# Performance work log

Hardware: AMD Instinct MI355X
Metric: run time of the kernel (lower is better)

Reference implementation:

```python
import jax, jax.numpy as jnp
import numpy as np

N_HIDDEN = 128
N_HEAD = 8
DIM_HEAD = N_HIDDEN // N_HEAD


def setup_inputs() -> dict:
    key = jax.random.key(0)
    ks = jax.random.split(key, 16)
    B, N, H = 2, 512, N_HIDDEN
    x = jax.random.normal(ks[0], (B, N, H), dtype=jnp.float32)
    e = jax.random.normal(ks[1], (B, N, N, H), dtype=jnp.float32)
    attention_mask = jnp.zeros((B, 1, N, N), dtype=jnp.float32)
    s = 1.0 / np.sqrt(H)
    def lin(kw, kb):
        W = jax.random.normal(kw, (H, H), dtype=jnp.float32) * s
        b = jax.random.normal(kb, (H,), dtype=jnp.float32) * s
        return W, b
    Wq, bq = lin(ks[2], ks[3])
    Wk, bk = lin(ks[4], ks[5])
    We, be = lin(ks[6], ks[7])
    Woh, boh = lin(ks[8], ks[9])
    Woe, boe = lin(ks[10], ks[11])
    return {"x": x, "e": e, "attention_mask": attention_mask,
            "Wq": Wq, "bq": bq, "Wk": Wk, "bk": bk,
            "We": We, "be": be, "Woh": Woh, "boh": boh,
            "Woe": Woe, "boe": boe}


def reference(x, e, attention_mask, Wq, bq, Wk, bk, We, be, Woh, boh, Woe, boe):
    B, N, H = x.shape
    h, dh = N_HEAD, DIM_HEAD
    # Projections -> [B, h, N, dh]
    Qx = (x @ Wq + bq).reshape(B, N, h, dh).transpose(0, 2, 1, 3)
    Kx = (x @ Wk + bk).reshape(B, N, h, dh).transpose(0, 2, 1, 3)
    Vx = Kx  # faithful to original: V_x = self.K(x)
    # Edge projection -> [B, h, N, N, dh]
    Ee = (e @ We + be).reshape(B, N, N, h, dh).transpose(0, 3, 1, 2, 4)
    # Elementwise Q*K*E biased scores: [B, h, N, N, dh]
    inter = Qx[:, :, :, None, :] * Kx[:, :, None, :, :] * Ee / np.sqrt(dh).astype(np.float32)
    scores = jax.nn.softmax(attention_mask + inter.sum(-1), axis=-1)  # [B, h, N, N]
    # Edge output: [B, N, N, H] -> Oe (dropout is identity at eval)
    e_out = inter.transpose(0, 2, 3, 1, 4).reshape(B, N, N, H) @ Woe + boe
    # Node output
    att = jnp.einsum('bhij,bhjd->bhid', scores, Vx)  # [B, h, N, dh]
    x_out = att.transpose(0, 2, 1, 3).reshape(B, N, H) @ Woh + boh
    return (x_out, e_out, scores)
```

## Files before the change

### kernel.cpp

```cpp
#include <hip/hip_runtime.h>
#include <hip/hip_bf16.h>


#define NB 2
#define NN 512
#define NHID 128
#define BQ 32

typedef __bf16 bf16x8 __attribute__((ext_vector_type(8)));
typedef __bf16 bf16x4 __attribute__((ext_vector_type(4)));
typedef float  f32x4  __attribute__((ext_vector_type(4)));
typedef float  vf4    __attribute__((ext_vector_type(4)));

union U16 { uint4 u; bf16x8 v; };

#define BAR_LGKM() do {                                          \
    asm volatile("s_waitcnt lgkmcnt(0)" ::: "memory");           \
    __builtin_amdgcn_sched_barrier(0);                           \
    __builtin_amdgcn_s_barrier();                                \
    __builtin_amdgcn_sched_barrier(0);                           \
} while (0)

__device__ __forceinline__ void swizzle_ib(int L, int& i, int& b) {
    const int Lp = (L & 7) * 128 + (L >> 3);
    b = Lp >> 9;
    i = Lp & 511;
}

__global__ __launch_bounds__(128)
void proj_kernel(const float* __restrict__ x,
                 const float* __restrict__ Wq, const float* __restrict__ bq,
                 const float* __restrict__ Wk, const float* __restrict__ bk,
                 float* __restrict__ Qhat, float* __restrict__ Khat)
{
    const int row = blockIdx.x;
    const int c   = threadIdx.x;
    __shared__ float xs[NHID];
    xs[c] = x[(long)row*NHID + c];
    __syncthreads();
    float q = bq[c], k = bk[c];
    #pragma unroll 8
    for (int kk = 0; kk < NHID; ++kk) {
        const float xv = xs[kk];
        q += xv * Wq[kk*NHID + c];
        k += xv * Wk[kk*NHID + c];
    }
    Qhat[(long)row*NHID + c] = q;
    Khat[(long)row*NHID + c] = k;
}

__global__ __launch_bounds__(128)
void wcvt_kernel(const float* __restrict__ We, const float* __restrict__ Woe,
                 __bf16* __restrict__ WeT, __bf16* __restrict__ WoeT)
{
    const int cb = blockIdx.x;
    const int k  = threadIdx.x;
    if (cb < NHID) {
        WeT[cb*NHID + k] = (__bf16)We[k*NHID + cb];
    } else {
        const int c = cb - NHID;
        WoeT[c*NHID + k] = (__bf16)Woe[k*NHID + c];
    }
}

__global__ __launch_bounds__(256, 4)
void mha_main(const float* __restrict__ e,
              const float* __restrict__ be,
              const float* __restrict__ boe,
              const float* __restrict__ Qhat,
              const float* __restrict__ Khat,
              const __bf16* __restrict__ WeT,
              const __bf16* __restrict__ WoeT,
              float* __restrict__ eout,
              float* __restrict__ sout)
{
    int i, b;
    swizzle_ib(blockIdx.y*NN + blockIdx.x, i, b);
    const int tid = threadIdx.x;
    const int w   = tid >> 6;
    const int l   = tid & 63;
    const int l15 = l & 15;
    const int lg  = l >> 4;
    const int wcol = w * 32;

    __shared__ __align__(16) __bf16 Elds[2][BQ*NHID];
    __shared__ __align__(16) __bf16 Mlds[BQ*NHID];

    const long rowbi = (long)b*NN + i;
    const float* Esrc = e    + rowbi*(long)(NN*NHID);
    float*       Edst = eout + rowbi*(long)(NN*NHID);
    const float* Kb   = Khat + (long)b*NN*NHID;

    float qv[2], bev[2], boev[2];
    bf16x8 fWe[2][4], fWoe[2][4];
    #pragma unroll
    for (int ct = 0; ct < 2; ++ct) {
        const int c = wcol + ct*16 + l15;
        qv[ct]   = Qhat[rowbi*NHID + c] * 0.25f;
        bev[ct]  = be[c];
        boev[ct] = boe[c];
        #pragma unroll
        for (int ks = 0; ks < 4; ++ks) {
            const int kb = ks*32 + lg*8;
            U16 ua, ub;
            ua.u = *(const uint4*)(WeT  + c*NHID + kb);
            ub.u = *(const uint4*)(WoeT + c*NHID + kb);
            fWe[ct][ks]  = ua.v;
            fWoe[ct][ks] = ub.v;
        }
    }
    const bool selp[4] = { (0*2 + (lg>>1)) == l15, (1*2 + (lg>>1)) == l15,
                           (2*2 + (lg>>1)) == l15, (3*2 + (lg>>1)) == l15 };

    vf4 rf[4];
    {
        const vf4* src = (const vf4*)Esrc;
        #pragma unroll
        for (int it = 0; it < 4; ++it)
            rf[it] = __builtin_nontemporal_load(&src[it*256 + tid]);
        #pragma unroll
        for (int it = 0; it < 4; ++it) {
            const int L = (it*256 + tid)*4;
            const int row = L >> 7, k = L & 127;
            bf16x4 v;
            v[0]=(__bf16)rf[it][0]; v[1]=(__bf16)rf[it][1];
            v[2]=(__bf16)rf[it][2]; v[3]=(__bf16)rf[it][3];
            *(bf16x4*)&Elds[0][row*NHID + (k ^ ((row&7)<<3))] = v;
        }
    }
    __syncthreads();

    for (int t = 0; t < 16; ++t) {
        const int cur = t & 1;
        if (t < 15) {
            const vf4* src = (const vf4*)(Esrc + (long)(t+1)*(BQ*NHID));
            #pragma unroll
            for (int it = 0; it < 4; ++it)
                rf[it] = __builtin_nontemporal_load(&src[it*256 + tid]);
        }

        f32x4 acc1[2][2] = {};
        #pragma unroll
        for (int ks = 0; ks < 4; ++ks) {
            bf16x8 fa[2];
            #pragma unroll
            for (int rt = 0; rt < 2; ++rt) {
                const int row = rt*16 + l15;
                fa[rt] = *(const bf16x8*)&Elds[cur][row*NHID + ((ks*32 + lg*8) ^ ((row&7)<<3))];
            }
            #pragma unroll
            for (int rt = 0; rt < 2; ++rt)
                #pragma unroll
                for (int ct = 0; ct < 2; ++ct)
                    acc1[rt][ct] = __builtin_amdgcn_mfma_f32_16x16x32_bf16(
                        fa[rt], fWe[ct][ks], acc1[rt][ct], 0, 0, 0);
        }

        #pragma unroll
        for (int rt = 0; rt < 2; ++rt)
            #pragma unroll
            for (int ct = 0; ct < 2; ++ct) {
                const int c = wcol + ct*16 + l15;
                #pragma unroll
                for (int rg = 0; rg < 4; ++rg) {
                    const int jl = rt*16 + lg*4 + rg;
                    const float ee  = acc1[rt][ct][rg] + bev[ct];
                    const float kvv = Kb[(long)(t*BQ + jl)*NHID + c];
                    const float m   = ee * qv[ct] * kvv;
                    Mlds[jl*NHID + (c ^ ((jl&7)<<3))] = (__bf16)m;
                }
            }

        BAR_LGKM();

        if (t < 15) {
            #pragma unroll
            for (int it = 0; it < 4; ++it) {
                const int L = (it*256 + tid)*4;
                const int row = L >> 7, k = L & 127;
                bf16x4 v;
                v[0]=(__bf16)rf[it][0]; v[1]=(__bf16)rf[it][1];
                v[2]=(__bf16)rf[it][2]; v[3]=(__bf16)rf[it][3];
                *(bf16x4*)&Elds[1-cur][row*NHID + (k ^ ((row&7)<<3))] = v;
            }
        }

        f32x4 acc2[2][2] = {};
        f32x4 accL[2] = {};
        #pragma unroll
        for (int ks = 0; ks < 4; ++ks) {
            bf16x8 fa[2];
            #pragma unroll
            for (int rt = 0; rt < 2; ++rt) {
                const int row = rt*16 + l15;
                fa[rt] = *(const bf16x8*)&Mlds[row*NHID + ((ks*32 + lg*8) ^ ((row&7)<<3))];
            }
            #pragma unroll
            for (int rt = 0; rt < 2; ++rt)
                #pragma unroll
                for (int ct = 0; ct < 2; ++ct)
                    acc2[rt][ct] = __builtin_amdgcn_mfma_f32_16x16x32_bf16(
                        fa[rt], fWoe[ct][ks], acc2[rt][ct], 0, 0, 0);
            if (w == 0) {
                U16 us;
                const unsigned ones = 0x3f803f80u;
                us.u.x = selp[ks] ? ones : 0u;
                us.u.y = us.u.x; us.u.z = us.u.x; us.u.w = us.u.x;
                #pragma unroll
                for (int rt = 0; rt < 2; ++rt)
                    accL[rt] = __builtin_amdgcn_mfma_f32_16x16x32_bf16(
                        fa[rt], us.v, accL[rt], 0, 0, 0);
            }
        }
        #pragma unroll
        for (int rt = 0; rt < 2; ++rt)
            #pragma unroll
            for (int ct = 0; ct < 2; ++ct) {
                const int c = wcol + ct*16 + l15;
                #pragma unroll
                for (int rg = 0; rg < 4; ++rg) {
                    const int jl = rt*16 + lg*4 + rg;
                    __builtin_nontemporal_store(acc2[rt][ct][rg] + boev[ct],
                                                &Edst[(long)(t*BQ + jl)*NHID + c]);
                }
            }
        if (w == 0 && l15 < 8) {
            float* lrow = sout + ((long)(b*8 + l15)*NN + i)*NN;
            #pragma unroll
            for (int rt = 0; rt < 2; ++rt)
                #pragma unroll
                for (int rg = 0; rg < 4; ++rg)
                    lrow[t*BQ + rt*16 + lg*4 + rg] = accL[rt][rg];
        }

        BAR_LGKM();
    }
}

__global__ __launch_bounds__(256)
void epilogue_kernel(const float* __restrict__ mask,
                     const float* __restrict__ Khat,
                     const float* __restrict__ Woh,
                     const float* __restrict__ boh,
                     float* __restrict__ xout,
                     float* __restrict__ sout)
{
    int i, b;
    swizzle_ib(blockIdx.y*NN + blockIdx.x, i, b);
    const int tid = threadIdx.x;
    const int w   = tid >> 6;
    const int l   = tid & 63;

    __shared__ float Llog[8][NN];
    __shared__ float AttP[2][NHID];
    __shared__ float AttF[NHID];

    const long rowbi = (long)b*NN + i;
    const float* mrow = mask + rowbi*NN;
    const float* Kb   = Khat + (long)b*NN*NHID;

    #pragma unroll
    for (int hh = 0; hh < 2; ++hh) {
        const int h = w*2 + hh;
        float* srow = sout + ((long)(b*8 + h)*NN + i)*NN;
        float vb[8];
        float mx = -1e30f;
        #pragma unroll
        for (int q = 0; q < 8; ++q) {
            const int j = q*64 + l;
            const float v = srow[j] + __builtin_nontemporal_load(&mrow[j]);
            vb[q] = v; mx = fmaxf(mx, v);
        }
        #pragma unroll
        for (int mm = 1; mm < 64; mm <<= 1) mx = fmaxf(mx, __shfl_xor(mx, mm));
        float sum = 0.f;
        #pragma unroll
        for (int q = 0; q < 8; ++q) { vb[q] = __expf(vb[q] - mx); sum += vb[q]; }
        #pragma unroll
        for (int mm = 1; mm < 64; mm <<= 1) sum += __shfl_xor(sum, mm);
        const float inv = 1.f / sum;
        #pragma unroll
        for (int q = 0; q < 8; ++q) {
            const int j = q*64 + l;
            const float p = vb[q]*inv;
            Llog[h][j] = p;
            srow[j] = p;
        }
    }
    __syncthreads();

    {
        const int half = tid >> 7;
        const int c = tid & 127;
        const int h = c >> 4;
        float a0 = 0.f, a1 = 0.f, a2 = 0.f, a3 = 0.f;
        const float* kp = Kb + (long)(half*256)*NHID + c;
        const float* pp = &Llog[h][half*256];
        #pragma unroll 4
        for (int j = 0; j < 256; j += 4) {
            a0 += pp[j]   * kp[(long)(j  )*NHID];
            a1 += pp[j+1] * kp[(long)(j+1)*NHID];
            a2 += pp[j+2] * kp[(long)(j+2)*NHID];
            a3 += pp[j+3] * kp[(long)(j+3)*NHID];
        }
        AttP[half][c] = (a0 + a1) + (a2 + a3);
    }
    __syncthreads();
    if (tid < NHID) AttF[tid] = AttP[0][tid] + AttP[1][tid];
    __syncthreads();

    if (tid < NHID) {
        const int c = tid;
        float a0 = boh[c], a1 = 0.f;
        #pragma unroll 8
        for (int k = 0; k < NHID; k += 2) {
            a0 += AttF[k]   * Woh[(k  )*NHID + c];
            a1 += AttF[k+1] * Woh[(k+1)*NHID + c];
        }
        xout[rowbi*NHID + c] = a0 + a1;
    }
}

extern "C" void kernel_launch(void* const* d_in, const int* in_sizes, int n_in,
                              void* d_out, int out_size, void* d_ws, size_t ws_size,
                              hipStream_t stream) {
    const float* x    = (const float*)d_in[0];
    const float* e    = (const float*)d_in[1];
    const float* mask = (const float*)d_in[2];
    const float* Wq   = (const float*)d_in[3];
    const float* bq   = (const float*)d_in[4];
    const float* Wk   = (const float*)d_in[5];
    const float* bk   = (const float*)d_in[6];
    const float* We   = (const float*)d_in[7];
    const float* be   = (const float*)d_in[8];
    const float* Woh  = (const float*)d_in[9];
    const float* boh  = (const float*)d_in[10];
    const float* Woe  = (const float*)d_in[11];
    const float* boe  = (const float*)d_in[12];

    float*  Qhat = (float*)d_ws;
    float*  Khat = Qhat + NB*NN*NHID;
    __bf16* WeT  = (__bf16*)(Khat + NB*NN*NHID);
    __bf16* WoeT = WeT + NHID*NHID;

    float* xout = (float*)d_out;
    float* eout = xout + (long)NB*NN*NHID;
    float* sout = eout + (long)NB*NN*NN*NHID;

    proj_kernel<<<dim3(NB*NN), 128, 0, stream>>>(x, Wq, bq, Wk, bk, Qhat, Khat);
    wcvt_kernel<<<dim3(2*NHID), 128, 0, stream>>>(We, Woe, WeT, WoeT);
    mha_main<<<dim3(NN, NB), 256, 0, stream>>>(e, be, boe, Qhat, Khat, WeT, WoeT,
                                               eout, sout);
    epilogue_kernel<<<dim3(NN, NB), 256, 0, stream>>>(mask, Khat, Woh, boh,
                                                      xout, sout);
}
```

Before: 359.4 us.

## Split main kernel j-range across two blocks, use bf16 K, plain stores

Each (b,i) row of the main kernel is now split into two halves of the j range, which doubles the grid so more blocks are available to fill the GPU. K is also stored as a bf16 copy to halve its gather traffic. The edge-output stores and mask loads switch from nontemporal to ordinary accesses. In exchange, each block repeats its weight-fragment and Q setup, and the K values used in the score product carry bf16 rounding.

Measured after the change: 402.9 us. 1.12x slower.

```diff
diff --git a/kernel.cpp b/kernel.cpp
--- a/kernel.cpp
+++ b/kernel.cpp
@@ -6,6 +6,7 @@
 #define NN 512
 #define NHID 128
 #define BQ 32
+#define TZH 8
 
 typedef __bf16 bf16x8 __attribute__((ext_vector_type(8)));
 typedef __bf16 bf16x4 __attribute__((ext_vector_type(4)));
@@ -21,17 +22,19 @@
     __builtin_amdgcn_sched_barrier(0);                           \
 } while (0)
 
-__device__ __forceinline__ void swizzle_ib(int L, int& i, int& b) {
-    const int Lp = (L & 7) * 128 + (L >> 3);
-    b = Lp >> 9;
-    i = Lp & 511;
+__device__ __forceinline__ void swizzle_ibt(int L, int& i, int& b, int& tz) {
+    const int Lp = (L & 7) * 256 + (L >> 3);
+    b  = Lp >> 10;
+    tz = (Lp >> 9) & 1;
+    i  = Lp & 511;
 }
 
 __global__ __launch_bounds__(128)
 void proj_kernel(const float* __restrict__ x,
                  const float* __restrict__ Wq, const float* __restrict__ bq,
                  const float* __restrict__ Wk, const float* __restrict__ bk,
-                 float* __restrict__ Qhat, float* __restrict__ Khat)
+                 float* __restrict__ Qhat, float* __restrict__ Khat,
+                 __bf16* __restrict__ KbT)
 {
     const int row = blockIdx.x;
     const int c   = threadIdx.x;
@@ -47,6 +50,7 @@
     }
     Qhat[(long)row*NHID + c] = q;
     Khat[(long)row*NHID + c] = k;
+    KbT [(long)row*NHID + c] = (__bf16)k;
 }
 
 __global__ __launch_bounds__(128)
@@ -68,28 +72,29 @@
               const float* __restrict__ be,
               const float* __restrict__ boe,
               const float* __restrict__ Qhat,
-              const float* __restrict__ Khat,
+              const __bf16* __restrict__ KbT,
               const __bf16* __restrict__ WeT,
               const __bf16* __restrict__ WoeT,
               float* __restrict__ eout,
               float* __restrict__ sout)
 {
-    int i, b;
-    swizzle_ib(blockIdx.y*NN + blockIdx.x, i, b);
+    int i, b, tz;
+    swizzle_ibt(blockIdx.y*NN + blockIdx.x, i, b, tz);
     const int tid = threadIdx.x;
     const int w   = tid >> 6;
     const int l   = tid & 63;
     const int l15 = l & 15;
     const int lg  = l >> 4;
     const int wcol = w * 32;
+    const int t0 = tz * TZH, t1 = t0 + TZH;
 
     __shared__ __align__(16) __bf16 Elds[2][BQ*NHID];
     __shared__ __align__(16) __bf16 Mlds[BQ*NHID];
 
     const long rowbi = (long)b*NN + i;
-    const float* Esrc = e    + rowbi*(long)(NN*NHID);
-    float*       Edst = eout + rowbi*(long)(NN*NHID);
-    const float* Kb   = Khat + (long)b*NN*NHID;
+    const float*  Esrc = e    + rowbi*(long)(NN*NHID);
+    float*        Edst = eout + rowbi*(long)(NN*NHID);
+    const __bf16* Kb   = KbT  + (long)b*NN*NHID;
 
     float qv[2], bev[2], boev[2];
     bf16x8 fWe[2][4], fWoe[2][4];
@@ -114,7 +119,7 @@
 
     vf4 rf[4];
     {
-        const vf4* src = (const vf4*)Esrc;
+        const vf4* src = (const vf4*)(Esrc + (long)t0*(BQ*NHID));
         #pragma unroll
         for (int it = 0; it < 4; ++it)
             rf[it] = __builtin_nontemporal_load(&src[it*256 + tid]);
@@ -130,9 +135,9 @@
     }
     __syncthreads();
 
-    for (int t = 0; t < 16; ++t) {
+    for (int t = t0; t < t1; ++t) {
         const int cur = t & 1;
-        if (t < 15) {
+        if (t < t1-1) {
             const vf4* src = (const vf4*)(Esrc + (long)(t+1)*(BQ*NHID));
             #pragma unroll
             for (int it = 0; it < 4; ++it)
@@ -165,7 +170,7 @@
                 for (int rg = 0; rg < 4; ++rg) {
                     const int jl = rt*16 + lg*4 + rg;
                     const float ee  = acc1[rt][ct][rg] + bev[ct];
-                    const float kvv = Kb[(long)(t*BQ + jl)*NHID + c];
+                    const float kvv = (float)Kb[(long)(t*BQ + jl)*NHID + c];
                     const float m   = ee * qv[ct] * kvv;
                     Mlds[jl*NHID + (c ^ ((jl&7)<<3))] = (__bf16)m;
                 }
@@ -173,7 +178,7 @@
 
         BAR_LGKM();
 
-        if (t < 15) {
+        if (t < t1-1) {
             #pragma unroll
             for (int it = 0; it < 4; ++it) {
                 const int L = (it*256 + tid)*4;
@@ -220,8 +225,7 @@
                 #pragma unroll
                 for (int rg = 0; rg < 4; ++rg) {
                     const int jl = rt*16 + lg*4 + rg;
-                    __builtin_nontemporal_store(acc2[rt][ct][rg] + boev[ct],
-                                                &Edst[(long)(t*BQ + jl)*NHID + c]);
+                    Edst[(long)(t*BQ + jl)*NHID + c] = acc2[rt][ct][rg] + boev[ct];
                 }
             }
         if (w == 0 && l15 < 8) {
@@ -245,8 +249,10 @@
                      float* __restrict__ xout,
                      float* __restrict__ sout)
 {
-    int i, b;
-    swizzle_ib(blockIdx.y*NN + blockIdx.x, i, b);
+    const int L = blockIdx.y*NN + blockIdx.x;
+    const int Lp = (L & 7) * 128 + (L >> 3);
+    const int b = Lp >> 9;
+    const int i = Lp & 511;
     const int tid = threadIdx.x;
     const int w   = tid >> 6;
     const int l   = tid & 63;
@@ -268,7 +274,7 @@
         #pragma unroll
         for (int q = 0; q < 8; ++q) {
             const int j = q*64 + l;
-            const float v = srow[j] + __builtin_nontemporal_load(&mrow[j]);
+            const float v = srow[j] + mrow[j];
             vb[q] = v; mx = fmaxf(mx, v);
         }
         #pragma unroll
@@ -342,15 +348,17 @@
     float*  Khat = Qhat + NB*NN*NHID;
     __bf16* WeT  = (__bf16*)(Khat + NB*NN*NHID);
     __bf16* WoeT = WeT + NHID*NHID;
+    __bf16* KbT  = WoeT + NHID*NHID;
 
     float* xout = (float*)d_out;
     float* eout = xout + (long)NB*NN*NHID;
     float* sout = eout + (long)NB*NN*NN*NHID;
 
-    proj_kernel<<<dim3(NB*NN), 128, 0, stream>>>(x, Wq, bq, Wk, bk, Qhat, Khat);
+    proj_kernel<<<dim3(NB*NN), 128, 0, stream>>>(x, Wq, bq, Wk, bk,
+                                                 Qhat, Khat, KbT);
     wcvt_kernel<<<dim3(2*NHID), 128, 0, stream>>>(We, Woe, WeT, WoeT);
-    mha_main<<<dim3(NN, NB), 256, 0, stream>>>(e, be, boe, Qhat, Khat, WeT, WoeT,
-                                               eout, sout);
+    mha_main<<<dim3(NN, 2*NB), 256, 0, stream>>>(e, be, boe, Qhat, KbT,
+                                                 WeT, WoeT, eout, sout);
     epilogue_kernel<<<dim3(NN, NB), 256, 0, stream>>>(mask, Khat, Woh, boh,
                                                       xout, sout);
 }
```
